# Kernel optimization log

Hardware: AMD Instinct MI355X
Metric: run time of the kernel (lower is better)

## Reference

```python
import jax, jax.numpy as jnp
import numpy as np

PATCH_SIZE = 7
EPS = 1e-6


def setup_inputs() -> dict:
    key = jax.random.key(0)
    k1, k2 = jax.random.split(key)
    pred = jax.random.uniform(k1, (8, 3, 512, 512), dtype=jnp.float32)
    gt = jax.random.uniform(k2, (8, 3, 512, 512), dtype=jnp.float32)
    return {"pred": pred, "gt": gt}


def _grayscale(x):
    # x: [B, 3, H, W] -> [B, H, W]
    return 0.299 * x[:, 0] + 0.587 * x[:, 1] + 0.114 * x[:, 2]


def reference(pred, gt):
    pred_g = _grayscale(pred.astype(jnp.float32))  # [B, H, W]
    gt_g = _grayscale(gt.astype(jnp.float32))
    B, H, W = pred_g.shape
    p = PATCH_SIZE
    pad = p // 2
    # zero padding matches F.unfold(padding=pad)
    pg = jnp.pad(pred_g, ((0, 0), (pad, pad), (pad, pad)))
    gg = jnp.pad(gt_g, ((0, 0), (pad, pad), (pad, pad)))
    # d_pred - d_gt = (patch_pred - center_pred) - (patch_gt - center_gt)
    # accumulate charbonnier sum over the p*p shifted views instead of
    # materializing the [B, p*p, H*W] unfold buffer
    total = jnp.zeros((), dtype=jnp.float32)
    for dy in range(p):
        for dx in range(p):
            sp = jax.lax.dynamic_slice(pg, (0, dy, dx), (B, H, W))
            sg = jax.lax.dynamic_slice(gg, (0, dy, dx), (B, H, W))
            d = (sp - pred_g) - (sg - gt_g)
            total = total + jnp.sum(jnp.sqrt(d * d + EPS))
    return total / (B * p * p * H * W)
```

## Files before the change

kernel.cpp:

```cpp
#include <hip/hip_runtime.h>


#define BB  8
#define HH  512
#define WW  512
#define HWP (HH * WW)
#define EPSF 1e-6f
#define PAD 3
#define TW  64
#define TH  32
#define LW  72
#define LHR (TH + 2 * PAD)
#define NU  (LHR * (LW / 4))
#define NBLK 1024

__global__ __launch_bounds__(256)
void census_fused_kernel(const float* __restrict__ pred,
                         const float* __restrict__ gt,
                         float* __restrict__ partials) {
    __shared__ float sh[LHR * LW];

    const int tid = threadIdx.x;
    const int bx = blockIdx.x;
    const int by = blockIdx.y;
    const int b  = blockIdx.z;

    const float* pr = pred + (size_t)b * 3 * HWP;
    const float* gr = gt   + (size_t)b * 3 * HWP;

    const int gx0 = bx * TW - 4;
    const int gy0 = by * TH - PAD;

    for (int i = tid; i < NU; i += 256) {
        const int r = i / (LW / 4);
        const int j = i - r * (LW / 4);
        const int gy = gy0 + r;
        const int gx = gx0 + 4 * j;
        float4 o = make_float4(0.f, 0.f, 0.f, 0.f);
        if ((unsigned)gy < (unsigned)HH && (unsigned)gx < (unsigned)WW) {
            const int off = gy * WW + gx;
            const float4 p0 = *(const float4*)(pr + off);
            const float4 p1 = *(const float4*)(pr + off + HWP);
            const float4 p2 = *(const float4*)(pr + off + 2 * HWP);
            const float4 g0 = *(const float4*)(gr + off);
            const float4 g1 = *(const float4*)(gr + off + HWP);
            const float4 g2 = *(const float4*)(gr + off + 2 * HWP);
            o.x = 0.299f * (p0.x - g0.x) + 0.587f * (p1.x - g1.x) + 0.114f * (p2.x - g2.x);
            o.y = 0.299f * (p0.y - g0.y) + 0.587f * (p1.y - g1.y) + 0.114f * (p2.y - g2.y);
            o.z = 0.299f * (p0.z - g0.z) + 0.587f * (p1.z - g1.z) + 0.114f * (p2.z - g2.z);
            o.w = 0.299f * (p0.w - g0.w) + 0.587f * (p1.w - g1.w) + 0.114f * (p2.w - g2.w);
        }
        *(float4*)(&sh[r * LW + 4 * j]) = o;
    }
    __syncthreads();

    const int lx  = tid & 63;
    const int ly0 = (tid >> 6) * 8;

    float c[8];
#pragma unroll
    for (int p = 0; p < 8; ++p)
        c[p] = sh[(ly0 + PAD + p) * LW + (lx + 4)];

    float av[4] = {0.f, 0.f, 0.f, 0.f};
#pragma unroll
    for (int dx = -3; dx <= 3; ++dx) {
        const int col = lx + 4 + dx;
        float s[11];
#pragma unroll
        for (int k = 0; k < 11; ++k)
            s[k] = sh[(ly0 + PAD + k) * LW + col];
        const int dy0 = (dx > 0) ? 0 : 1;
#pragma unroll
        for (int p = 0; p < 8; ++p) {
#pragma unroll
            for (int dy = dy0; dy <= 3; ++dy) {
                const float d = s[p + dy] - c[p];
                av[p & 3] += __builtin_amdgcn_sqrtf(fmaf(d, d, EPSF));
            }
        }
    }
    float acc2 = (av[0] + av[1]) + (av[2] + av[3]);

    float corr = 0.f;
    if (bx == 0 || bx == (WW / TW - 1) || by == 0 || by == (HH / TH - 1)) {
        const int xx = bx * TW + lx;
        const int bw = min(3, xx) + min(3, WW - 1 - xx) + 1;
        const int e  = max(0, 3 - xx) - max(0, xx - (WW - 4));
#pragma unroll
        for (int p = 0; p < 8; ++p) {
            const int y  = by * TH + ly0 + p;
            const int a  = min(3, HH - 1 - y);
            const int ap = min(3, y);
            const int w  = bw * (a - ap) + e;
            if (w != 0)
                corr += (float)w * __builtin_amdgcn_sqrtf(fmaf(c[p], c[p], EPSF));
        }
    }

    float acc = fmaf(2.f, acc2, corr);

#pragma unroll
    for (int off = 32; off > 0; off >>= 1)
        acc += __shfl_down(acc, off);

    __shared__ float wsum[4];
    if ((tid & 63) == 0) wsum[tid >> 6] = acc;
    __syncthreads();
    if (tid == 0) {
        const float s = (wsum[0] + wsum[1]) + (wsum[2] + wsum[3])
                      + (float)(TW * TH) * __builtin_amdgcn_sqrtf(EPSF);
        const int bid = (b * 16 + by) * 8 + bx;
        partials[bid] = s;
    }
}

__global__ __launch_bounds__(256)
void census_reduce_kernel(const float* __restrict__ partials,
                          float* __restrict__ out) {
    const int tid = threadIdx.x;
    float acc = (partials[tid] + partials[tid + 256])
              + (partials[tid + 512] + partials[tid + 768]);
#pragma unroll
    for (int off = 32; off > 0; off >>= 1)
        acc += __shfl_down(acc, off);
    __shared__ float wsum[4];
    if ((tid & 63) == 0) wsum[tid >> 6] = acc;
    __syncthreads();
    if (tid == 0) {
        const float s = (wsum[0] + wsum[1]) + (wsum[2] + wsum[3]);
        const float scale = (float)(1.0 / ((double)BB * 49.0 * HH * WW));
        out[0] = s * scale;
    }
}

extern "C" void kernel_launch(void* const* d_in, const int* in_sizes, int n_in,
                              void* d_out, int out_size, void* d_ws, size_t ws_size,
                              hipStream_t stream) {
    const float* pred = (const float*)d_in[0];
    const float* gt   = (const float*)d_in[1];
    float* out = (float*)d_out;
    float* partials = (float*)d_ws;

    const dim3 grid(WW / TW, HH / TH, BB);
    census_fused_kernel<<<grid, 256, 0, stream>>>(pred, gt, partials);
    census_reduce_kernel<<<1, 256, 0, stream>>>(partials, out);
}
```

Before: 96.68 us.

## Process two 64x64 tiles per block with register-prefetched double buffering

Replaces the 1024-block kernel (64x32 tiles, 256 threads) with 256 blocks of 512 threads. Each block handles two adjacent 64x64 tiles and prefetches the second tile's global loads into registers while computing the first from shared memory. The goal is to hide global-load latency and cut per-block halo overhead. The costs are 36 float4 registers held per thread for the staged data, which lowers occupancy, and only 256 blocks, which may underfill the GPU's compute units.

```diff
diff --git a/kernel.cpp b/kernel.cpp
--- a/kernel.cpp
+++ b/kernel.cpp
@@ -7,69 +7,80 @@
 #define HWP (HH * WW)
 #define EPSF 1e-6f
 #define PAD 3
-#define TW  64
-#define TH  32
+#define TS  64
 #define LW  72
-#define LHR (TH + 2 * PAD)
-#define NU  (LHR * (LW / 4))
-#define NBLK 1024
+#define LH  70
+#define UNITS (LH * (LW/4))
+#define NTHR 512
+#define NBLK 256
 
-__global__ __launch_bounds__(256)
-void census_fused_kernel(const float* __restrict__ pred,
-                         const float* __restrict__ gt,
-                         float* __restrict__ partials) {
-    __shared__ float sh[LHR * LW];
-
-    const int tid = threadIdx.x;
-    const int bx = blockIdx.x;
-    const int by = blockIdx.y;
-    const int b  = blockIdx.z;
-
-    const float* pr = pred + (size_t)b * 3 * HWP;
-    const float* gr = gt   + (size_t)b * 3 * HWP;
-
-    const int gx0 = bx * TW - 4;
-    const int gy0 = by * TH - PAD;
-
-    for (int i = tid; i < NU; i += 256) {
-        const int r = i / (LW / 4);
-        const int j = i - r * (LW / 4);
+__device__ __forceinline__ void stage_load(const float* __restrict__ pr,
+                                           const float* __restrict__ gr,
+                                           int gx0, int gy0, int tid,
+                                           float4 (&P)[3][3], float4 (&G)[3][3],
+                                           bool (&inb)[3]) {
+#pragma unroll
+    for (int it = 0; it < 3; ++it) {
+        const int u = tid + it * NTHR;
+        const int r = u / 18;
+        const int j = u - r * 18;
         const int gy = gy0 + r;
         const int gx = gx0 + 4 * j;
-        float4 o = make_float4(0.f, 0.f, 0.f, 0.f);
-        if ((unsigned)gy < (unsigned)HH && (unsigned)gx < (unsigned)WW) {
+        bool ok = (u < UNITS) && ((unsigned)gy < (unsigned)HH)
+                               && ((unsigned)gx < (unsigned)WW);
+        inb[it] = ok;
+        if (ok) {
             const int off = gy * WW + gx;
-            const float4 p0 = *(const float4*)(pr + off);
-            const float4 p1 = *(const float4*)(pr + off + HWP);
-            const float4 p2 = *(const float4*)(pr + off + 2 * HWP);
-            const float4 g0 = *(const float4*)(gr + off);
-            const float4 g1 = *(const float4*)(gr + off + HWP);
-            const float4 g2 = *(const float4*)(gr + off + 2 * HWP);
-            o.x = 0.299f * (p0.x - g0.x) + 0.587f * (p1.x - g1.x) + 0.114f * (p2.x - g2.x);
-            o.y = 0.299f * (p0.y - g0.y) + 0.587f * (p1.y - g1.y) + 0.114f * (p2.y - g2.y);
-            o.z = 0.299f * (p0.z - g0.z) + 0.587f * (p1.z - g1.z) + 0.114f * (p2.z - g2.z);
-            o.w = 0.299f * (p0.w - g0.w) + 0.587f * (p1.w - g1.w) + 0.114f * (p2.w - g2.w);
+#pragma unroll
+            for (int ch = 0; ch < 3; ++ch) {
+                P[it][ch] = *(const float4*)(pr + off + ch * HWP);
+                G[it][ch] = *(const float4*)(gr + off + ch * HWP);
+            }
         }
-        *(float4*)(&sh[r * LW + 4 * j]) = o;
     }
-    __syncthreads();
+}
 
+__device__ __forceinline__ void stage_write(float* __restrict__ shbuf, int tid,
+                                            const float4 (&P)[3][3],
+                                            const float4 (&G)[3][3],
+                                            const bool (&inb)[3]) {
+#pragma unroll
+    for (int it = 0; it < 3; ++it) {
+        const int u = tid + it * NTHR;
+        if (u < UNITS) {
+            const int r = u / 18;
+            const int j = u - r * 18;
+            float4 o = make_float4(0.f, 0.f, 0.f, 0.f);
+            if (inb[it]) {
+                o.x = 0.299f * (P[it][0].x - G[it][0].x) + 0.587f * (P[it][1].x - G[it][1].x) + 0.114f * (P[it][2].x - G[it][2].x);
+                o.y = 0.299f * (P[it][0].y - G[it][0].y) + 0.587f * (P[it][1].y - G[it][1].y) + 0.114f * (P[it][2].y - G[it][2].y);
+                o.z = 0.299f * (P[it][0].z - G[it][0].z) + 0.587f * (P[it][1].z - G[it][1].z) + 0.114f * (P[it][2].z - G[it][2].z);
+                o.w = 0.299f * (P[it][0].w - G[it][0].w) + 0.587f * (P[it][1].w - G[it][1].w) + 0.114f * (P[it][2].w - G[it][2].w);
+            }
+            *(float4*)(shbuf + r * LW + 4 * j) = o;
+        }
+    }
+}
+
+__device__ __forceinline__ float tile_compute(const float* __restrict__ shbuf,
+                                              int tid, int tx, int ty) {
     const int lx  = tid & 63;
-    const int ly0 = (tid >> 6) * 8;
+    const int w   = tid >> 6;
+    const int ly0 = w * 8;
 
     float c[8];
 #pragma unroll
     for (int p = 0; p < 8; ++p)
-        c[p] = sh[(ly0 + PAD + p) * LW + (lx + 4)];
+        c[p] = shbuf[(PAD + ly0 + p) * LW + 4 + lx];
 
     float av[4] = {0.f, 0.f, 0.f, 0.f};
 #pragma unroll
     for (int dx = -3; dx <= 3; ++dx) {
-        const int col = lx + 4 + dx;
+        const int col = 4 + lx + dx;
         float s[11];
 #pragma unroll
         for (int k = 0; k < 11; ++k)
-            s[k] = sh[(ly0 + PAD + k) * LW + col];
+            s[k] = shbuf[(ly0 + PAD + k) * LW + col];
         const int dy0 = (dx > 0) ? 0 : 1;
 #pragma unroll
         for (int p = 0; p < 8; ++p) {
@@ -83,35 +94,65 @@
     float acc2 = (av[0] + av[1]) + (av[2] + av[3]);
 
     float corr = 0.f;
-    if (bx == 0 || bx == (WW / TW - 1) || by == 0 || by == (HH / TH - 1)) {
-        const int xx = bx * TW + lx;
+    if (tx == 0 || tx == (WW / TS - 1) || ty == 0 || ty == (HH / TS - 1)) {
+        const int xx = tx * TS + lx;
         const int bw = min(3, xx) + min(3, WW - 1 - xx) + 1;
         const int e  = max(0, 3 - xx) - max(0, xx - (WW - 4));
 #pragma unroll
         for (int p = 0; p < 8; ++p) {
-            const int y  = by * TH + ly0 + p;
+            const int y  = ty * TS + ly0 + p;
             const int a  = min(3, HH - 1 - y);
             const int ap = min(3, y);
-            const int w  = bw * (a - ap) + e;
-            if (w != 0)
-                corr += (float)w * __builtin_amdgcn_sqrtf(fmaf(c[p], c[p], EPSF));
+            const int wgt = bw * (a - ap) + e;
+            if (wgt != 0)
+                corr += (float)wgt * __builtin_amdgcn_sqrtf(fmaf(c[p], c[p], EPSF));
         }
     }
+    return fmaf(2.f, acc2, corr);
+}
 
-    float acc = fmaf(2.f, acc2, corr);
+__global__ __launch_bounds__(NTHR)
+void census_persist_kernel(const float* __restrict__ pred,
+                           const float* __restrict__ gt,
+                           float* __restrict__ partials) {
+    __shared__ float sh[2][LH * LW];
+
+    const int tid = threadIdx.x;
+    const int t0  = blockIdx.x * 2;
+    const int tx0 = t0 & 7;
+    const int ty  = (t0 >> 3) & 7;
+    const int b   = t0 >> 6;
+    const int tx1 = tx0 + 1;
+
+    const float* pr = pred + (size_t)b * 3 * HWP;
+    const float* gr = gt   + (size_t)b * 3 * HWP;
+
+    float4 P0[3][3], G0[3][3]; bool i0[3];
+    stage_load(pr, gr, tx0 * TS - 4, ty * TS - PAD, tid, P0, G0, i0);
+    stage_write(sh[0], tid, P0, G0, i0);
+    __syncthreads();
+
+    float4 P1[3][3], G1[3][3]; bool i1[3];
+    stage_load(pr, gr, tx1 * TS - 4, ty * TS - PAD, tid, P1, G1, i1);
+
+    float acc = tile_compute(sh[0], tid, tx0, ty);
+
+    stage_write(sh[1], tid, P1, G1, i1);
+    __syncthreads();
+
+    acc += tile_compute(sh[1], tid, tx1, ty);
 
 #pragma unroll
     for (int off = 32; off > 0; off >>= 1)
         acc += __shfl_down(acc, off);
-
-    __shared__ float wsum[4];
+    __shared__ float wsum[8];
     if ((tid & 63) == 0) wsum[tid >> 6] = acc;
     __syncthreads();
     if (tid == 0) {
-        const float s = (wsum[0] + wsum[1]) + (wsum[2] + wsum[3])
-                      + (float)(TW * TH) * __builtin_amdgcn_sqrtf(EPSF);
-        const int bid = (b * 16 + by) * 8 + bx;
-        partials[bid] = s;
+        float s = 0.f;
+#pragma unroll
+        for (int i = 0; i < 8; ++i) s += wsum[i];
+        partials[blockIdx.x] = s;
     }
 }
 
@@ -119,8 +160,7 @@
 void census_reduce_kernel(const float* __restrict__ partials,
                           float* __restrict__ out) {
     const int tid = threadIdx.x;
-    float acc = (partials[tid] + partials[tid + 256])
-              + (partials[tid + 512] + partials[tid + 768]);
+    float acc = partials[tid];
 #pragma unroll
     for (int off = 32; off > 0; off >>= 1)
         acc += __shfl_down(acc, off);
@@ -128,7 +168,8 @@
     if ((tid & 63) == 0) wsum[tid >> 6] = acc;
     __syncthreads();
     if (tid == 0) {
-        const float s = (wsum[0] + wsum[1]) + (wsum[2] + wsum[3]);
+        const float s = (wsum[0] + wsum[1]) + (wsum[2] + wsum[3])
+                      + (float)((double)BB * HH * WW) * __builtin_amdgcn_sqrtf(EPSF);
         const float scale = (float)(1.0 / ((double)BB * 49.0 * HH * WW));
         out[0] = s * scale;
     }
@@ -142,7 +183,6 @@
     float* out = (float*)d_out;
     float* partials = (float*)d_ws;
 
-    const dim3 grid(WW / TW, HH / TH, BB);
-    census_fused_kernel<<<grid, 256, 0, stream>>>(pred, gt, partials);
+    census_persist_kernel<<<NBLK, NTHR, 0, stream>>>(pred, gt, partials);
     census_reduce_kernel<<<1, 256, 0, stream>>>(partials, out);
 }
```

Result: no change. 96.44 us (-0.3%).
